# Performance work log

Hardware: AMD Instinct MI355X
Metric: run time of the kernel (lower is better)

Reference implementation:

```python
import jax, jax.numpy as jnp
import numpy as np

B, C, IN, H = 64, 128, 1024, 512  # batch, channels, input features (=='seq_length' arg), hidden


def setup_inputs() -> dict:
    key = jax.random.key(0)
    ks = jax.random.split(key, 9)
    s = 1.0 / np.sqrt(H)  # PyTorch LSTM init: U(-1/sqrt(H), 1/sqrt(H))
    u = lambda k, shape: jax.random.uniform(k, shape, jnp.float32, -s, s)
    return {
        "x": jax.random.normal(ks[0], (B, C, IN), jnp.float32),
        # layer 0: one weight set per direction (fwd, bwd)
        "W_ih0": u(ks[1], (2, 4 * H, IN)),
        "W_hh0": u(ks[2], (2, 4 * H, H)),
        "b_ih0": u(ks[3], (2, 4 * H)),
        "b_hh0": u(ks[4], (2, 4 * H)),
        # layers 1..2: input is concat of both directions (2H)
        "W_ih12": u(ks[5], (2, 2, 4 * H, 2 * H)),
        "W_hh12": u(ks[6], (2, 2, 4 * H, H)),
        "b_ih12": u(ks[7], (2, 2, 4 * H)),
        "b_hh12": u(ks[8], (2, 2, 4 * H)),
    }


def _cell(inp, W_ih, b_ih, b_hh):
    # One LSTM step from zero state (h0 = c0 = 0): W_hh @ h0 == 0, f*c0 == 0.
    gates = inp @ W_ih.T + b_ih + b_hh  # [N, 4H]
    i, f, g, o = jnp.split(gates, 4, axis=-1)  # PyTorch gate order: i, f, g, o
    c = jax.nn.sigmoid(i) * jnp.tanh(g)
    return jax.nn.sigmoid(o) * jnp.tanh(c)  # h, shape [N, H]


def reference(x, W_ih0, W_hh0, b_ih0, b_hh0, W_ih12, W_hh12, b_ih12, b_hh12):
    b, c, n = x.shape
    # Each channel is an independent seq-len-1 LSTM call with zero init state,
    # so fold channels into the batch dimension. W_hh* contribute nothing (h0=0).
    xb = x.reshape(b * c, n)
    h = jnp.concatenate(
        [_cell(xb, W_ih0[d], b_ih0[d], b_hh0[d]) for d in range(2)], axis=-1
    )  # [b*c, 2H]
    for l in range(2):  # layers 1 and 2
        h = jnp.concatenate(
            [_cell(h, W_ih12[l, d], b_ih12[l, d], b_hh12[l, d]) for d in range(2)],
            axis=-1,
        )
    return h.reshape(b, c, 2 * H)  # [batch, channels, 2*hidden]
```

## Files before the change

### kernel.cpp

```cpp
#include <hip/hip_runtime.h>


typedef float f32x4 __attribute__((ext_vector_type(4)));
typedef short short8 __attribute__((ext_vector_type(8)));
typedef unsigned short u16;

#define NP 3072
#define MROWS 8192
#define KDIM 1024
#define BM 128
#define BN 96
#define BK 32
#define LDS_TILE 14336

__device__ __forceinline__ u16 f2bf(float f) {
  unsigned u = __float_as_uint(f);
  u += 0x7fffu + ((u >> 16) & 1u);
  return (u16)(u >> 16);
}
__device__ __forceinline__ float sigmoid_f(float x) {
  return 1.0f / (1.0f + __expf(-x));
}
__device__ __forceinline__ float tanh_f(float x) {
  float xc = fminf(fmaxf(x, -15.0f), 15.0f);
  float e = __expf(2.0f * xc);
  return (e - 1.0f) / (e + 1.0f);
}
__device__ __forceinline__ void gload_lds16(const void* g, void* l) {
  __builtin_amdgcn_global_load_lds((const __attribute__((address_space(1))) void*)g,
                                   (__attribute__((address_space(3))) void*)l,
                                   16, 0, 0);
}


__global__ __launch_bounds__(256) void k_convert_x(const float* __restrict__ x,
                                                   u16* __restrict__ out) {
  int tid = blockIdx.x * 256 + threadIdx.x;
  const float4* src = (const float4*)x + (size_t)tid * 2;
  float4 v0 = src[0], v1 = src[1];
  union { u16 u[8]; uint4 v; } r;
  r.u[0] = f2bf(v0.x); r.u[1] = f2bf(v0.y); r.u[2] = f2bf(v0.z); r.u[3] = f2bf(v0.w);
  r.u[4] = f2bf(v1.x); r.u[5] = f2bf(v1.y); r.u[6] = f2bf(v1.z); r.u[7] = f2bf(v1.w);
  ((uint4*)out)[tid] = r.v;
}

__global__ __launch_bounds__(256) void k_pack_w(const float* __restrict__ Wih0,
                                                const float* __restrict__ Wih12,
                                                u16* __restrict__ P) {
  int tid = blockIdx.x * 256 + threadIdx.x;
  int s   = tid / (NP * 128);
  int rem = tid - s * (NP * 128);
  int p   = rem >> 7;
  int k8  = rem & 127;
  int hb = p / 48;
  int pr = p - hb * 48;
  int gs = pr >> 4;
  int hl = pr & 15;
  int hcol = hb * 16 + hl;
  int dir = hcol >> 9;
  int h   = hcol & 511;
  int og  = (gs == 0) ? 0 : (gs + 1);
  const float* src;
  if (s == 0)
    src = Wih0 + ((size_t)(dir * 2048 + og * 512 + h)) * 1024 + k8 * 8;
  else
    src = Wih12 + ((size_t)(((s - 1) * 2 + dir) * 2048 + og * 512 + h)) * 1024 + k8 * 8;
  float4 v0 = ((const float4*)src)[0];
  float4 v1 = ((const float4*)src)[1];
  union { u16 u[8]; uint4 v; } r;
  r.u[0] = f2bf(v0.x); r.u[1] = f2bf(v0.y); r.u[2] = f2bf(v0.z); r.u[3] = f2bf(v0.w);
  r.u[4] = f2bf(v1.x); r.u[5] = f2bf(v1.y); r.u[6] = f2bf(v1.z); r.u[7] = f2bf(v1.w);
  ((uint4*)P)[tid] = r.v;
}

__global__ __launch_bounds__(256) void k_pack_bias(const float* __restrict__ bih0,
                                                   const float* __restrict__ bhh0,
                                                   const float* __restrict__ bih12,
                                                   const float* __restrict__ bhh12,
                                                   float* __restrict__ pb) {
  int tid = blockIdx.x * 256 + threadIdx.x;
  if (tid >= 3 * NP) return;
  int s = tid / NP;
  int p = tid - s * NP;
  int hb = p / 48;
  int pr = p - hb * 48;
  int gs = pr >> 4;
  int hl = pr & 15;
  int hcol = hb * 16 + hl;
  int dir = hcol >> 9;
  int h   = hcol & 511;
  int og  = (gs == 0) ? 0 : (gs + 1);
  int j   = og * 512 + h;
  float v;
  if (s == 0) {
    int i = dir * 2048 + j;
    v = bih0[i] + bhh0[i];
  } else {
    int i = ((s - 1) * 2 + dir) * 2048 + j;
    v = bih12[i] + bhh12[i];
  }
  pb[tid] = v;
}


#define MM(Macc, Aop, Bop) Macc = __builtin_amdgcn_mfma_f32_16x16x32_bf16(Aop, Bop, Macc, 0, 0, 0)

#define STAGE(BUF, KT) \
  gload_lds16(srcA + (size_t)(KT) * BK,              lds + (BUF) * LDS_TILE + t * 16); \
  gload_lds16(srcA + 64 * KDIM + (size_t)(KT) * BK,  lds + (BUF) * LDS_TILE + 4096 + t * 16); \
  gload_lds16(srcB + (size_t)(KT) * BK,              lds + (BUF) * LDS_TILE + 8192 + t * 16); \
  if (t < 128) { gload_lds16(srcB + 64 * KDIM + (size_t)(KT) * BK, lds + (BUF) * LDS_TILE + 12288 + t * 16); }

#define KSTEP(BUF, KT, DOST) \
  { \
    if (DOST) { STAGE((BUF)^1, (KT)+1); } \
    const char* base = lds + (BUF) * LDS_TILE; \
    short8 a0 = *(const short8*)(base + aOff); \
    short8 a1 = *(const short8*)(base + aOff + 1024); \
    short8 a2 = *(const short8*)(base + aOff + 2048); \
    short8 a3 = *(const short8*)(base + aOff + 3072); \
    short8 b0 = *(const short8*)(base + bOff); \
    short8 b1 = *(const short8*)(base + bOff + 1024); \
    short8 b2 = *(const short8*)(base + bOff + 2048); \
    MM(acc[0][0], a0, b0); MM(acc[1][0], a1, b0); MM(acc[2][0], a2, b0); MM(acc[3][0], a3, b0); \
    MM(acc[0][1], a0, b1); MM(acc[1][1], a1, b1); MM(acc[2][1], a2, b1); MM(acc[3][1], a3, b1); \
    MM(acc[0][2], a0, b2); MM(acc[1][2], a1, b2); MM(acc[2][2], a2, b2); MM(acc[3][2], a3, b2); \
    __syncthreads(); \
  }

template <bool F32OUT>
__global__ __launch_bounds__(256, 4) void k_lstm_gemm97(const u16* __restrict__ A,
                                                        const u16* __restrict__ Bp,
                                                        const float* __restrict__ bias,
                                                        void* __restrict__ outp) {
  __shared__ __align__(16) char lds[2 * LDS_TILE];
  const int t    = threadIdx.x;
  const int lane = t & 63;
  const int w    = t >> 6;
  const int wr   = w >> 1;
  const int wc   = w & 1;
  const int r16  = lane & 15, kg = lane >> 4;

  const int n_hw = blockIdx.y * gridDim.x + blockIdx.x;
  const int c    = n_hw & 7;
  const int wlc  = n_hw >> 3;
  const int bx   = (c & 1) * 16 + (wlc & 15);
  const int by   = (c >> 1) * 16 + (wlc >> 4);
  const int brow = by * BM;
  const int bn0  = bx * BN;

  const int sw   = (r16 >> 1) & 3;
  const int slot = (kg ^ sw) << 4;
  const int aOff = wr * 4096 + r16 * 64 + slot;
  const int bOff = 8192 + wc * 3072 + r16 * 64 + slot;

  const int srow = t >> 2;
  const int koct = ((t & 3) ^ ((t >> 3) & 3)) << 3;
  const u16* srcA = A  + (size_t)(brow + srow) * KDIM + koct;
  const u16* srcB = Bp + (size_t)(bn0  + srow) * KDIM + koct;

  f32x4 acc[4][3];
#pragma unroll
  for (int m = 0; m < 4; ++m)
#pragma unroll
    for (int n = 0; n < 3; ++n) acc[m][n] = (f32x4){0.f, 0.f, 0.f, 0.f};

  STAGE(0, 0);
  __syncthreads();

  for (int k2 = 0; k2 < 15; ++k2) {
    KSTEP(0, 2 * k2, 1);
    KSTEP(1, 2 * k2 + 1, 1);
  }
  KSTEP(0, 30, 1);
  KSTEP(1, 31, 0);

  {
    int pbase = bn0 + wc * 48;
    float biV = bias[pbase + r16];
    float bgV = bias[pbase + 16 + r16];
    float boV = bias[pbase + 32 + r16];
    int hcol = (2 * bx + wc) * 16 + r16;
#pragma unroll
    for (int m = 0; m < 4; ++m) {
      int rowb = brow + wr * 64 + m * 16 + kg * 4;
#pragma unroll
      for (int r = 0; r < 4; ++r) {
        float vi = acc[m][0][r] + biV;
        float vg = acc[m][1][r] + bgV;
        float vo = acc[m][2][r] + boV;
        float c2 = sigmoid_f(vi) * tanh_f(vg);
        float hv = sigmoid_f(vo) * tanh_f(c2);
        size_t oidx = (size_t)(rowb + r) * 1024 + hcol;
        if (F32OUT) ((float*)outp)[oidx] = hv;
        else        ((u16*)outp)[oidx]   = f2bf(hv);
      }
    }
  }
}

extern "C" void kernel_launch(void* const* d_in, const int* in_sizes, int n_in,
                              void* d_out, int out_size, void* d_ws, size_t ws_size,
                              hipStream_t stream) {
  const float* x     = (const float*)d_in[0];
  const float* Wih0  = (const float*)d_in[1];
  const float* bih0  = (const float*)d_in[3];
  const float* bhh0  = (const float*)d_in[4];
  const float* Wih12 = (const float*)d_in[5];
  const float* bih12 = (const float*)d_in[7];
  const float* bhh12 = (const float*)d_in[8];

  char* ws = (char*)d_ws;
  u16*   xbf = (u16*)ws;
  u16*   h1  = (u16*)(ws + 16777216);
  u16*   h2  = (u16*)(ws + 33554432);
  u16*   P3  = (u16*)(ws + 50331648);
  float* pb3 = (float*)(ws + 69206016);

  k_convert_x<<<4096, 256, 0, stream>>>(x, xbf);
  k_pack_w<<<4608, 256, 0, stream>>>(Wih0, Wih12, P3);
  k_pack_bias<<<36, 256, 0, stream>>>(bih0, bhh0, bih12, bhh12, pb3);

  dim3 grid(NP / BN, MROWS / BM);
  k_lstm_gemm97<false><<<grid, 256, 0, stream>>>(xbf, P3, pb3, h1);
  k_lstm_gemm97<false><<<grid, 256, 0, stream>>>(h1, P3 + (size_t)NP * KDIM, pb3 + NP, h2);
  k_lstm_gemm97<true ><<<grid, 256, 0, stream>>>(h2, P3 + (size_t)2 * NP * KDIM, pb3 + 2 * NP, d_out);
}
```

Measured before the change: 233.0 us.

## Triple-buffer LDS tiles with partial vmcnt waits and MFMA priority boost

Moves the GEMM main loop from double to triple buffering, so global-to-LDS loads are issued two k-steps ahead. The full __syncthreads is replaced with a partial s_waitcnt vmcnt plus a raw barrier, so only the older tile's loads must land before the barrier. It also raises wave priority around the MFMA block. The extra LDS buffer lowers the launch-bound occupancy from 4 to 3 blocks per CU. The hand-counted vmcnt values depend on the exact number of loads each thread issues per stage.

```diff
diff --git a/kernel.cpp b/kernel.cpp
--- a/kernel.cpp
+++ b/kernel.cpp
@@ -103,6 +103,9 @@
 }
 
 
+#define BAR()    __builtin_amdgcn_s_barrier()
+#define SCHEDB() __builtin_amdgcn_sched_barrier(0)
+#define WAITV(N) asm volatile("s_waitcnt vmcnt(" #N ")" ::: "memory")
 #define MM(Macc, Aop, Bop) Macc = __builtin_amdgcn_mfma_f32_16x16x32_bf16(Aop, Bop, Macc, 0, 0, 0)
 
 #define STAGE(BUF, KT) \
@@ -111,10 +114,10 @@
   gload_lds16(srcB + (size_t)(KT) * BK,              lds + (BUF) * LDS_TILE + 8192 + t * 16); \
   if (t < 128) { gload_lds16(srcB + 64 * KDIM + (size_t)(KT) * BK, lds + (BUF) * LDS_TILE + 12288 + t * 16); }
 
-#define KSTEP(BUF, KT, DOST) \
+#define KSTEP(RBUF, SBUF, KT, DOST, LASTT) \
   { \
-    if (DOST) { STAGE((BUF)^1, (KT)+1); } \
-    const char* base = lds + (BUF) * LDS_TILE; \
+    if (DOST) { STAGE(SBUF, (KT) + 2); } \
+    const char* base = lds + (RBUF) * LDS_TILE; \
     short8 a0 = *(const short8*)(base + aOff); \
     short8 a1 = *(const short8*)(base + aOff + 1024); \
     short8 a2 = *(const short8*)(base + aOff + 2048); \
@@ -122,18 +125,22 @@
     short8 b0 = *(const short8*)(base + bOff); \
     short8 b1 = *(const short8*)(base + bOff + 1024); \
     short8 b2 = *(const short8*)(base + bOff + 2048); \
+    __builtin_amdgcn_s_setprio(1); \
     MM(acc[0][0], a0, b0); MM(acc[1][0], a1, b0); MM(acc[2][0], a2, b0); MM(acc[3][0], a3, b0); \
     MM(acc[0][1], a0, b1); MM(acc[1][1], a1, b1); MM(acc[2][1], a2, b1); MM(acc[3][1], a3, b1); \
     MM(acc[0][2], a0, b2); MM(acc[1][2], a1, b2); MM(acc[2][2], a2, b2); MM(acc[3][2], a3, b2); \
-    __syncthreads(); \
+    __builtin_amdgcn_s_setprio(0); \
+    if (DOST) { if (t < 128) { WAITV(4); } else { WAITV(3); } } \
+    else if (!(LASTT)) { WAITV(0); } \
+    if (!(LASTT)) { BAR(); SCHEDB(); } \
   }
 
 template <bool F32OUT>
-__global__ __launch_bounds__(256, 4) void k_lstm_gemm97(const u16* __restrict__ A,
+__global__ __launch_bounds__(256, 3) void k_lstm_gemm97(const u16* __restrict__ A,
                                                         const u16* __restrict__ Bp,
                                                         const float* __restrict__ bias,
                                                         void* __restrict__ outp) {
-  __shared__ __align__(16) char lds[2 * LDS_TILE];
+  __shared__ __align__(16) char lds[3 * LDS_TILE];
   const int t    = threadIdx.x;
   const int lane = t & 63;
   const int w    = t >> 6;
@@ -166,14 +173,18 @@
     for (int n = 0; n < 3; ++n) acc[m][n] = (f32x4){0.f, 0.f, 0.f, 0.f};
 
   STAGE(0, 0);
-  __syncthreads();
-
-  for (int k2 = 0; k2 < 15; ++k2) {
-    KSTEP(0, 2 * k2, 1);
-    KSTEP(1, 2 * k2 + 1, 1);
-  }
-  KSTEP(0, 30, 1);
-  KSTEP(1, 31, 0);
+  STAGE(1, 1);
+  if (t < 128) { WAITV(4); } else { WAITV(3); }
+  BAR(); SCHEDB();
+
+  for (int k3 = 0; k3 < 10; ++k3) {
+    int kt = k3 * 3;
+    KSTEP(0, 2, kt + 0, 1, 0);
+    KSTEP(1, 0, kt + 1, 1, 0);
+    KSTEP(2, 1, kt + 2, 1, 0);
+  }
+  KSTEP(0, 0, 30, 0, 0);
+  KSTEP(1, 0, 31, 0, 1);
 
   {
     int pbase = bn0 + wc * 48;
```

New measurement: 232.2 us. About the same (-0.4%).
